# Kernel optimization log

Hardware: AMD Instinct MI355X
Metric: run time of the kernel (lower is better)

The kernel has to match this reference:

```python
import jax, jax.numpy as jnp
import numpy as np

N_PTS = 1_000_000
N_CORNERS = 2_000_000  # per-level corner count (table has +1 zero row for misses)
FEAT_DIM = 16
MAX_LEVEL = 12
FEAT_LEVELS = 3  # levels MAX_LEVEL, MAX_LEVEL-1, MAX_LEVEL-2
POLY_INT = True


def setup_inputs() -> dict:
    key = jax.random.key(0)
    ks = jax.random.split(key, 8)
    x = jax.random.uniform(ks[0], (N_PTS, 3), jnp.float32, -1.0, 1.0)
    std = 0.05
    feats = [std * jax.random.normal(ks[1 + i], (N_CORNERS + 1, FEAT_DIM), jnp.float32)
             for i in range(FEAT_LEVELS)]
    # last row is the zero feature for unobserved nodes
    feats = [f.at[-1].set(0.0) for f in feats]
    idxs = [jax.random.randint(ks[4 + i], (N_PTS, 8), 0, N_CORNERS, dtype=jnp.int64)
            for i in range(FEAT_LEVELS)]
    return {"x": x,
            "feat0": feats[0], "feat1": feats[1], "feat2": feats[2],
            "idx0": idxs[0], "idx1": idxs[1], "idx2": idxs[2]}


def _interp_coeffs(x, level, polynomial_on=POLY_INT):
    # coords = 2^level * (x*0.5 + 0.5); d = frac(coords)
    coords = (2.0 ** level) * (x * 0.5 + 0.5)
    d = coords - jnp.floor(coords)                      # [N,3]
    t = 3.0 * d**2 - 2.0 * d**3 if polynomial_on else d
    tx, ty, tz = t[:, 0], t[:, 1], t[:, 2]
    ux, uy, uz = 1.0 - tx, 1.0 - ty, 1.0 - tz
    # corner order matches torch.stack((p0..p7)): z fastest, then y, then x
    p = jnp.stack([ux * uy * uz, ux * uy * tz, ux * ty * uz, ux * ty * tz,
                   tx * uy * uz, tx * uy * tz, tx * ty * uz, tx * ty * tz],
                  axis=1)                               # [N,8]
    return p


def reference(x, feat0, feat1, feat2, idx0, idx1, idx2):
    feats = (feat0, feat1, feat2)
    idxs = (idx0, idx1, idx2)
    out = jnp.zeros((x.shape[0], FEAT_DIM), dtype=x.dtype)
    for i in range(FEAT_LEVELS):
        level = MAX_LEVEL - i
        p = _interp_coeffs(x, level)                    # [N,8]
        g = feats[i][idxs[i]]                           # [N,8,D] gather
        out = out + jnp.einsum("nk,nkd->nd", p, g)
    return out
```

## Files before the change

### kernel.cpp

```cpp
#include <hip/hip_runtime.h>


__device__ __forceinline__ void accum_level(
    long long pt, int sub, float cx, float cy, float cz,
    const float4* __restrict__ feat, const int* __restrict__ idx,
    float4& acc)
{
    float dx = cx - floorf(cx);
    float dy = cy - floorf(cy);
    float dz = cz - floorf(cz);
    float tx = dx * dx * (3.0f - 2.0f * dx);
    float ty = dy * dy * (3.0f - 2.0f * dy);
    float tz = dz * dz * (3.0f - 2.0f * dz);
    float ux = 1.0f - tx, uy = 1.0f - ty, uz = 1.0f - tz;

    float p[8];
    p[0] = ux * uy * uz;
    p[1] = ux * uy * tz;
    p[2] = ux * ty * uz;
    p[3] = ux * ty * tz;
    p[4] = tx * uy * uz;
    p[5] = tx * uy * tz;
    p[6] = tx * ty * uz;
    p[7] = tx * ty * tz;

    const int4* iv = (const int4*)(idx + pt * 8);
    int4 ia = iv[0];
    int4 ib = iv[1];
    int id[8] = { ia.x, ia.y, ia.z, ia.w, ib.x, ib.y, ib.z, ib.w };

#pragma unroll
    for (int k = 0; k < 8; ++k) {
        float4 g = feat[(long long)id[k] * 4 + sub];
        acc.x = fmaf(p[k], g.x, acc.x);
        acc.y = fmaf(p[k], g.y, acc.y);
        acc.z = fmaf(p[k], g.z, acc.z);
        acc.w = fmaf(p[k], g.w, acc.w);
    }
}

__global__ __launch_bounds__(256) void FeatureOctree_74749610820348_kernel(
    const float* __restrict__ x,
    const float4* __restrict__ f0,
    const float4* __restrict__ f1,
    const float4* __restrict__ f2,
    const int* __restrict__ i0,
    const int* __restrict__ i1,
    const int* __restrict__ i2,
    float4* __restrict__ out,
    int n_pts)
{
    long long tid = (long long)blockIdx.x * blockDim.x + threadIdx.x;
    long long pt = tid >> 2;
    int sub = (int)(tid & 3);
    if (pt >= n_pts) return;

    float xv = x[pt * 3 + 0];
    float yv = x[pt * 3 + 1];
    float zv = x[pt * 3 + 2];

    float bx = xv * 0.5f + 0.5f;
    float by = yv * 0.5f + 0.5f;
    float bz = zv * 0.5f + 0.5f;

    float4 acc = make_float4(0.f, 0.f, 0.f, 0.f);

    accum_level(pt, sub, 4096.0f * bx, 4096.0f * by, 4096.0f * bz, f0, i0, acc);
    accum_level(pt, sub, 2048.0f * bx, 2048.0f * by, 2048.0f * bz, f1, i1, acc);
    accum_level(pt, sub, 1024.0f * bx, 1024.0f * by, 1024.0f * bz, f2, i2, acc);

    out[pt * 4 + sub] = acc;
}

extern "C" void kernel_launch(void* const* d_in, const int* in_sizes, int n_in,
                              void* d_out, int out_size, void* d_ws, size_t ws_size,
                              hipStream_t stream) {
    const float*  x  = (const float*)d_in[0];
    const float4* f0 = (const float4*)d_in[1];
    const float4* f1 = (const float4*)d_in[2];
    const float4* f2 = (const float4*)d_in[3];
    const int*    i0 = (const int*)d_in[4];
    const int*    i1 = (const int*)d_in[5];
    const int*    i2 = (const int*)d_in[6];
    float4* out = (float4*)d_out;

    int n_pts = in_sizes[0] / 3;
    long long total = (long long)n_pts * 4;
    int block = 256;
    int grid = (int)((total + block - 1) / block);

    FeatureOctree_74749610820348_kernel<<<grid, block, 0, stream>>>(
        x, f0, f1, f2, i0, i1, i2, out, n_pts);
}
```

Baseline: 780.7 us.

## Split octree interpolation into per-level kernel launches with nontemporal streaming accesses

Replaces the single fused kernel, which gathered from all three feature tables, with three launches of a templated kernel that each handle one level. The first launch writes the output and the later two read it back and add to it. The goal is for only one feature table's gathers to compete for the last-level cache at a time, and nontemporal loads and stores on x, the indices and the output keep that streaming data from evicting gathered rows. The cost is re-reading x, an extra read and write of the output per level, and two more kernel launches.

After: 796.3 us. 1.02x slower.

```diff
diff --git a/kernel.cpp b/kernel.cpp
--- a/kernel.cpp
+++ b/kernel.cpp
@@ -1,11 +1,31 @@
 #include <hip/hip_runtime.h>
 
 
-__device__ __forceinline__ void accum_level(
-    long long pt, int sub, float cx, float cy, float cz,
-    const float4* __restrict__ feat, const int* __restrict__ idx,
-    float4& acc)
+typedef float v4f __attribute__((ext_vector_type(4)));
+typedef int   v4i __attribute__((ext_vector_type(4)));
+
+template <bool ACCUM>
+__global__ __launch_bounds__(256) void octree_level_kernel(
+    const float* __restrict__ x,
+    const v4f* __restrict__ feat,
+    const int* __restrict__ idx,
+    v4f* __restrict__ out,
+    float scale,
+    int n_pts)
 {
+    long long tid = (long long)blockIdx.x * blockDim.x + threadIdx.x;
+    long long pt = tid >> 2;
+    int sub = (int)(tid & 3);
+    if (pt >= n_pts) return;
+
+    float xv = __builtin_nontemporal_load(x + pt * 3 + 0);
+    float yv = __builtin_nontemporal_load(x + pt * 3 + 1);
+    float zv = __builtin_nontemporal_load(x + pt * 3 + 2);
+
+    float cx = scale * (xv * 0.5f + 0.5f);
+    float cy = scale * (yv * 0.5f + 0.5f);
+    float cz = scale * (zv * 0.5f + 0.5f);
+
     float dx = cx - floorf(cx);
     float dy = cy - floorf(cy);
     float dz = cz - floorf(cz);
@@ -24,71 +44,48 @@
     p[6] = tx * ty * uz;
     p[7] = tx * ty * tz;
 
-    const int4* iv = (const int4*)(idx + pt * 8);
-    int4 ia = iv[0];
-    int4 ib = iv[1];
+    const v4i* iv = (const v4i*)(idx + pt * 8);
+    v4i ia = __builtin_nontemporal_load(iv);
+    v4i ib = __builtin_nontemporal_load(iv + 1);
     int id[8] = { ia.x, ia.y, ia.z, ia.w, ib.x, ib.y, ib.z, ib.w };
+
+    v4f acc;
+    if (ACCUM) {
+        acc = __builtin_nontemporal_load(out + pt * 4 + sub);
+    } else {
+        acc = (v4f){0.0f, 0.0f, 0.0f, 0.0f};
+    }
 
 #pragma unroll
     for (int k = 0; k < 8; ++k) {
-        float4 g = feat[(long long)id[k] * 4 + sub];
+        v4f g = feat[(long long)id[k] * 4 + sub];
         acc.x = fmaf(p[k], g.x, acc.x);
         acc.y = fmaf(p[k], g.y, acc.y);
         acc.z = fmaf(p[k], g.z, acc.z);
         acc.w = fmaf(p[k], g.w, acc.w);
     }
-}
 
-__global__ __launch_bounds__(256) void FeatureOctree_74749610820348_kernel(
-    const float* __restrict__ x,
-    const float4* __restrict__ f0,
-    const float4* __restrict__ f1,
-    const float4* __restrict__ f2,
-    const int* __restrict__ i0,
-    const int* __restrict__ i1,
-    const int* __restrict__ i2,
-    float4* __restrict__ out,
-    int n_pts)
-{
-    long long tid = (long long)blockIdx.x * blockDim.x + threadIdx.x;
-    long long pt = tid >> 2;
-    int sub = (int)(tid & 3);
-    if (pt >= n_pts) return;
-
-    float xv = x[pt * 3 + 0];
-    float yv = x[pt * 3 + 1];
-    float zv = x[pt * 3 + 2];
-
-    float bx = xv * 0.5f + 0.5f;
-    float by = yv * 0.5f + 0.5f;
-    float bz = zv * 0.5f + 0.5f;
-
-    float4 acc = make_float4(0.f, 0.f, 0.f, 0.f);
-
-    accum_level(pt, sub, 4096.0f * bx, 4096.0f * by, 4096.0f * bz, f0, i0, acc);
-    accum_level(pt, sub, 2048.0f * bx, 2048.0f * by, 2048.0f * bz, f1, i1, acc);
-    accum_level(pt, sub, 1024.0f * bx, 1024.0f * by, 1024.0f * bz, f2, i2, acc);
-
-    out[pt * 4 + sub] = acc;
+    __builtin_nontemporal_store(acc, out + pt * 4 + sub);
 }
 
 extern "C" void kernel_launch(void* const* d_in, const int* in_sizes, int n_in,
                               void* d_out, int out_size, void* d_ws, size_t ws_size,
                               hipStream_t stream) {
-    const float*  x  = (const float*)d_in[0];
-    const float4* f0 = (const float4*)d_in[1];
-    const float4* f1 = (const float4*)d_in[2];
-    const float4* f2 = (const float4*)d_in[3];
-    const int*    i0 = (const int*)d_in[4];
-    const int*    i1 = (const int*)d_in[5];
-    const int*    i2 = (const int*)d_in[6];
-    float4* out = (float4*)d_out;
+    const float* x  = (const float*)d_in[0];
+    const v4f*   f0 = (const v4f*)d_in[1];
+    const v4f*   f1 = (const v4f*)d_in[2];
+    const v4f*   f2 = (const v4f*)d_in[3];
+    const int*   i0 = (const int*)d_in[4];
+    const int*   i1 = (const int*)d_in[5];
+    const int*   i2 = (const int*)d_in[6];
+    v4f* out = (v4f*)d_out;
 
     int n_pts = in_sizes[0] / 3;
     long long total = (long long)n_pts * 4;
     int block = 256;
     int grid = (int)((total + block - 1) / block);
 
-    FeatureOctree_74749610820348_kernel<<<grid, block, 0, stream>>>(
-        x, f0, f1, f2, i0, i1, i2, out, n_pts);
+    octree_level_kernel<false><<<grid, block, 0, stream>>>(x, f0, i0, out, 4096.0f, n_pts);
+    octree_level_kernel<true ><<<grid, block, 0, stream>>>(x, f1, i1, out, 2048.0f, n_pts);
+    octree_level_kernel<true ><<<grid, block, 0, stream>>>(x, f2, i2, out, 1024.0f, n_pts);
 }
```
